# Kernel optimization log

Measured on AMD Instinct MI355X. Metric: run time of the kernel, lower is better.

Reference implementation:

```python
import jax, jax.numpy as jnp
import numpy as np

H = 128; NC = 100000; ND = 20000; NG = 50000; E = 150000; EP = 100000; L = 2

def _ln(x, g, b, eps=1e-5):
    mu = jnp.mean(x, -1, keepdims=True)
    v = jnp.mean((x - mu) ** 2, -1, keepdims=True)
    return (x - mu) * jax.lax.rsqrt(v + eps) * g + b

def _gelu(x):
    return jax.nn.gelu(x, approximate=False)  # torch nn.GELU default = exact erf

def _sage(x_src, x_dst, ei, Wl, bl, Wr):
    # PyG SAGEConv: mean-aggregate src features over incoming edges, lin_l(agg)+bias + lin_r(x_dst)
    n_dst = x_dst.shape[0]
    msg = x_src[ei[0]]                                   # [E, H] gather
    s = jax.ops.segment_sum(msg, ei[1], num_segments=n_dst)
    cnt = jax.ops.segment_sum(jnp.ones((ei.shape[1],), x_src.dtype), ei[1], num_segments=n_dst)
    agg = s / jnp.maximum(cnt, 1.0)[:, None]             # zero for isolated dst nodes
    return agg @ Wl + bl + x_dst @ Wr

def _make_ei(k, ns, nd, e):
    k1, k2 = jax.random.split(k)
    return jnp.stack([jax.random.randint(k1, (e,), 0, ns, dtype=jnp.int32),
                      jax.random.randint(k2, (e,), 0, nd, dtype=jnp.int32)])

def setup_inputs() -> dict:
    key = jax.random.key(0)
    ks = jax.random.split(key, 16)
    s = 0.05
    return {
        "x_chem": jax.random.normal(ks[0], (NC, 128), jnp.float32),
        "x_dis": jax.random.normal(ks[1], (ND, 128), jnp.float32),
        "gene_emb": jax.random.normal(ks[2], (NG, H), jnp.float32) * s,
        "proj_W": jax.random.normal(ks[3], (2, 128, H), jnp.float32) * s,
        "proj_b": jnp.zeros((2, H), jnp.float32),
        "proj_ln_g": jnp.ones((2, H), jnp.float32),
        "proj_ln_b": jnp.zeros((2, H), jnp.float32),
        "sage_Wl": jax.random.normal(ks[4], (L, 4, H, H), jnp.float32) * s,
        "sage_bl": jnp.zeros((L, 4, H), jnp.float32),
        "sage_Wr": jax.random.normal(ks[5], (L, 4, H, H), jnp.float32) * s,
        "ln_g": jnp.ones((L, 3, H), jnp.float32),
        "ln_b": jnp.zeros((L, 3, H), jnp.float32),
        "W_cd": jax.random.normal(ks[6], (H, H), jnp.float32) * s,
        "ei_c2d": _make_ei(ks[7], NC, ND, E),
        "ei_d2c": _make_ei(ks[8], ND, NC, E),
        "ei_c2g": _make_ei(ks[9], NC, NG, E),
        "ei_g2c": _make_ei(ks[10], NG, NC, E),
        "pos_edge": _make_ei(ks[11], NC, ND, EP),
        "neg_edge": _make_ei(ks[12], NC, ND, EP),
    }

def reference(x_chem, x_dis, gene_emb, proj_W, proj_b, proj_ln_g, proj_ln_b,
              sage_Wl, sage_bl, sage_Wr, ln_g, ln_b, W_cd,
              ei_c2d, ei_d2c, ei_c2g, ei_g2c, pos_edge, neg_edge):
    # init node states: Linear+LN+GELU for featured ntypes, embedding table for gene
    hc = _gelu(_ln(x_chem @ proj_W[0] + proj_b[0], proj_ln_g[0], proj_ln_b[0]))
    hd = _gelu(_ln(x_dis @ proj_W[1] + proj_b[1], proj_ln_g[1], proj_ln_b[1]))
    hg = gene_emb
    for l in range(L):
        # HeteroConv aggr='mean': chemical receives d2c (idx1) and g2c (idx3) -> mean of 2
        nc = 0.5 * (_sage(hd, hc, ei_d2c, sage_Wl[l, 1], sage_bl[l, 1], sage_Wr[l, 1])
                    + _sage(hg, hc, ei_g2c, sage_Wl[l, 3], sage_bl[l, 3], sage_Wr[l, 3]))
        nd = _sage(hc, hd, ei_c2d, sage_Wl[l, 0], sage_bl[l, 0], sage_Wr[l, 0])
        ng = _sage(hc, hg, ei_c2g, sage_Wl[l, 2], sage_bl[l, 2], sage_Wr[l, 2])
        # residual + LN + GELU (dropout is identity in eval mode)
        hc = _gelu(_ln(nc + hc, ln_g[l, 0], ln_b[l, 0]))
        hd = _gelu(_ln(nd + hd, ln_g[l, 1], ln_b[l, 1]))
        hg = _gelu(_ln(ng + hg, ln_g[l, 2], ln_b[l, 2]))
    def dec(ei):
        return ((hc[ei[0]] @ W_cd) * hd[ei[1]]).sum(-1)
    return dec(pos_edge), dec(neg_edge)
```

## Files before the change

### kernel.cpp

```cpp
#include <hip/hip_runtime.h>

#define HD 128

constexpr int T_NC = 100000;
constexpr int T_ND = 20000;
constexpr int T_NG = 50000;
constexpr int T_E  = 150000;
constexpr int T_EP = 100000;
constexpr int NMAT = 21;
constexpr int DEGN = 2 * T_NC + T_ND + T_NG;

typedef __attribute__((ext_vector_type(8))) short   s16x8;
typedef __attribute__((ext_vector_type(8))) __bf16  bf16x8;
typedef __attribute__((ext_vector_type(4))) float   f32x4;

union Frag { s16x8 s; bf16x8 b; };

__device__ __forceinline__ float gelu_f(float x) {
    return 0.5f * x * (1.0f + erff(x * 0.70710678118654752f));
}

__global__ void pack_weights(const float* __restrict__ proj_W,
                             const float* __restrict__ sage_Wl,
                             const float* __restrict__ sage_Wr,
                             const float* __restrict__ W_cd,
                             unsigned short* __restrict__ phi,
                             unsigned short* __restrict__ plo)
{
    int m = blockIdx.x;
    const float* W;
    const float* W2 = nullptr;
    if (m < 2)        W = proj_W  + (size_t)m * HD * HD;
    else if (m < 10)  W = sage_Wl + (size_t)(m - 2) * HD * HD;
    else if (m < 18)  W = sage_Wr + (size_t)(m - 10) * HD * HD;
    else if (m == 18) W = W_cd;
    else {
        int l = m - 19;
        W  = sage_Wr + (size_t)(l * 4 + 1) * HD * HD;
        W2 = sage_Wr + (size_t)(l * 4 + 3) * HD * HD;
    }

    int t = threadIdx.x;
    int kstep = t >> 6;
    int lane  = t & 63;
    int kbase = kstep * 32 + (lane >> 4) * 8;
    int c     = lane & 15;
    for (int cb = 0; cb < 8; ++cb) {
        int col = cb * 16 + c;
        size_t off = ((((size_t)m * 8 + cb) * 4 + kstep) * 64 + lane) * 8;
        #pragma unroll
        for (int j = 0; j < 8; ++j) {
            float w = W[(size_t)(kbase + j) * HD + col];
            if (W2) w += W2[(size_t)(kbase + j) * HD + col];
            __bf16 h = (__bf16)w;
            union { __bf16 b; unsigned short u; } ch, cl;
            ch.b = h;
            cl.b = (__bf16)(w - (float)h);
            phi[off + j] = ch.u;
            plo[off + j] = cl.u;
        }
    }
}

__global__ void conv_gene(const float* __restrict__ src, unsigned short* __restrict__ dst)
{
    size_t i = (size_t)(blockIdx.x * blockDim.x + threadIdx.x) * 8;
    if (i >= (size_t)T_NG * HD) return;
    f32x4 a0 = *(const f32x4*)(src + i);
    f32x4 a1 = *(const f32x4*)(src + i + 4);
    Frag u;
    u.b[0] = (__bf16)a0.x; u.b[1] = (__bf16)a0.y; u.b[2] = (__bf16)a0.z; u.b[3] = (__bf16)a0.w;
    u.b[4] = (__bf16)a1.x; u.b[5] = (__bf16)a1.y; u.b[6] = (__bf16)a1.z; u.b[7] = (__bf16)a1.w;
    *(s16x8*)(dst + i) = u.s;
}

__global__ void edge_count4(const int* __restrict__ eA, const int* __restrict__ eB,
                            const int* __restrict__ eC, const int* __restrict__ eD,
                            int gPer, int* __restrict__ deg)
{
    int seg = blockIdx.x / gPer;
    int e = (blockIdx.x % gPer) * 256 + threadIdx.x;
    if (e >= T_E) return;
    const int* ei = seg == 0 ? eA : seg == 1 ? eB : seg == 2 ? eC : eD;
    int off = seg == 0 ? 0 : seg == 1 ? T_NC : seg == 2 ? 2 * T_NC : 2 * T_NC + T_ND;
    atomicAdd(&deg[off + ei[T_E + e]], 1);
}

__global__ void scan_local(const int* __restrict__ deg, int* __restrict__ rp,
                           int* __restrict__ bsum, int N)
{
    __shared__ int wtot[4];
    int t = threadIdx.x;
    int lane = t & 63, w = t >> 6;
    int base = blockIdx.x * 1024 + t * 4;
    int v[4];
    #pragma unroll
    for (int j = 0; j < 4; ++j) v[j] = (base + j < N) ? deg[base + j] : 0;
    int p1 = v[0] + v[1];
    int p2 = p1 + v[2];
    int total = p2 + v[3];
    int sc = total;
    #pragma unroll
    for (int o = 1; o < 64; o <<= 1) {
        int y = __shfl_up(sc, o);
        if (lane >= o) sc += y;
    }
    if (lane == 63) wtot[w] = sc;
    __syncthreads();
    int woff = 0;
    for (int i = 0; i < w; ++i) woff += wtot[i];
    int ex = woff + sc - total;
    if (base + 0 < N) rp[base + 0] = ex;
    if (base + 1 < N) rp[base + 1] = ex + v[0];
    if (base + 2 < N) rp[base + 2] = ex + p1;
    if (base + 3 < N) rp[base + 3] = ex + p2;
    if (t == 255) bsum[blockIdx.x] = woff + sc;
}

__global__ void scan_tops(int* __restrict__ bsum, int B)
{
    int lane = threadIdx.x;
    int off = 0;
    for (int s = 0; s < B; s += 64) {
        int i = s + lane;
        int v = (i < B) ? bsum[i] : 0;
        int sc = v;
        #pragma unroll
        for (int o = 1; o < 64; o <<= 1) {
            int y = __shfl_up(sc, o);
            if (lane >= o) sc += y;
        }
        if (i < B) bsum[i] = off + sc - v;
        off += __shfl(sc, 63);
    }
}

__global__ void scan_add(int* __restrict__ rp, const int* __restrict__ bsum, int N)
{
    int base = blockIdx.x * 1024 + threadIdx.x * 4;
    int o = bsum[blockIdx.x];
    #pragma unroll
    for (int j = 0; j < 4; ++j)
        if (base + j < N) rp[base + j] += o;
}

__global__ void edge_fill4(const int* __restrict__ eA, const int* __restrict__ eB,
                           const int* __restrict__ eC, const int* __restrict__ eD,
                           int gPer, const int* __restrict__ rp,
                           int* __restrict__ fil, int* __restrict__ col)
{
    int seg = blockIdx.x / gPer;
    int e = (blockIdx.x % gPer) * 256 + threadIdx.x;
    if (e >= T_E) return;
    const int* ei = seg == 0 ? eA : seg == 1 ? eB : seg == 2 ? eC : eD;
    int off = seg == 0 ? 0 : seg == 1 ? T_NC : seg == 2 ? 2 * T_NC : 2 * T_NC + T_ND;
    int d = ei[T_E + e];
    int p = rp[off + d] + atomicAdd(&fil[off + d], 1);
    col[p] = ei[e];
}

struct Pair {
    const void* A;
    const int* rp; const int* dg; const int* col;
    int w; int fmt;
};
struct Seg {
    Pair p0, p1, p2;
    const float *bias0, *bias1, *g_ln, *b_ln;
    unsigned short* out;
    float scale;
    int np, use_res, M, nblk;
};

template<int MODE>
__global__ __launch_bounds__(256, 8)
void fused_gemm(Seg s0, Seg s1, Seg s2,
                const unsigned short* __restrict__ phi,
                const unsigned short* __restrict__ plo)
{
    __shared__ __align__(16) unsigned short As_hi[32 * HD];
    __shared__ __align__(16) unsigned short As_lo[32 * HD];
    __shared__ float psum[4][32];
    __shared__ float psq[4][32];

    int bid = blockIdx.x;
    Seg s;
    if (bid < s0.nblk) s = s0;
    else if (bid < s0.nblk + s1.nblk) { bid -= s0.nblk; s = s1; }
    else { bid -= s0.nblk + s1.nblk; s = s2; }

    const int tid  = threadIdx.x;
    const int w    = tid >> 6;
    const int lane = tid & 63;
    const int c    = lane & 15;
    const int hi4  = lane >> 4;
    const int row0 = bid * 32;

    f32x4 acc[2][2];
    #pragma unroll
    for (int rb = 0; rb < 2; ++rb)
        #pragma unroll
        for (int q = 0; q < 2; ++q) acc[rb][q] = (f32x4)0.f;

    for (int p = 0; p < s.np; ++p) {
        Pair P = (p == 0) ? s.p0 : (p == 1) ? s.p1 : s.p2;
        const bool gath = (P.rp != nullptr);

        __syncthreads();
        for (int it = 0; it < 2; ++it) {
            int u  = tid + it * 256;
            int r  = u >> 4;
            int k8 = (u & 15) * 8;
            int gr = row0 + r;
            Frag vh, vl;
            vh.s = (s16x8)0; vl.s = (s16x8)0;
            if (gr < s.M) {
                if (gath) {
                    float av[8] = {0.f, 0.f, 0.f, 0.f, 0.f, 0.f, 0.f, 0.f};
                    int st = P.rp[gr];
                    int d  = P.dg[gr];
                    const unsigned short* Ah = (const unsigned short*)P.A;
                    int i = 0;
                    for (; i + 2 <= d; i += 2) {
                        int e0 = P.col[st + i];
                        int e1 = P.col[st + i + 1];
                        Frag x0, x1;
                        x0.s = *(const s16x8*)(Ah + (size_t)e0 * HD + k8);
                        x1.s = *(const s16x8*)(Ah + (size_t)e1 * HD + k8);
                        #pragma unroll
                        for (int j = 0; j < 8; ++j)
                            av[j] += (float)x0.b[j] + (float)x1.b[j];
                    }
                    if (i < d) {
                        int e0 = P.col[st + i];
                        Frag x0;
                        x0.s = *(const s16x8*)(Ah + (size_t)e0 * HD + k8);
                        #pragma unroll
                        for (int j = 0; j < 8; ++j)
                            av[j] += (float)x0.b[j];
                    }
                    float rs = 1.f / (float)(d > 1 ? d : 1);
                    #pragma unroll
                    for (int j = 0; j < 8; ++j) {
                        float x = av[j] * rs;
                        __bf16 h = (__bf16)x;
                        vh.b[j] = h;
                        vl.b[j] = (__bf16)(x - (float)h);
                    }
                } else if (P.fmt) {
                    vh.s = *(const s16x8*)((const unsigned short*)P.A + (size_t)gr * HD + k8);
                } else {
                    const f32x4* ap = (const f32x4*)((const float*)P.A + (size_t)gr * HD + k8);
                    f32x4 a0 = ap[0], a1 = ap[1];
                    vh.b[0] = (__bf16)a0.x; vh.b[1] = (__bf16)a0.y;
                    vh.b[2] = (__bf16)a0.z; vh.b[3] = (__bf16)a0.w;
                    vh.b[4] = (__bf16)a1.x; vh.b[5] = (__bf16)a1.y;
                    vh.b[6] = (__bf16)a1.z; vh.b[7] = (__bf16)a1.w;
                }
            }
            int sidx = (r * HD + k8) ^ ((r & 7) << 3);
            *(s16x8*)(As_hi + sidx) = vh.s;
            if (gath) *(s16x8*)(As_lo + sidx) = vl.s;
        }
        __syncthreads();

        #pragma unroll
        for (int ks = 0; ks < 4; ++ks) {
            Frag bh[2], bl[2];
            #pragma unroll
            for (int q = 0; q < 2; ++q) {
                int cbG = w * 2 + q;
                size_t boff = ((((size_t)P.w * 8 + cbG) * 4 + ks) * 64 + lane) * 8;
                bh[q].s = *(const s16x8*)(phi + boff);
                bl[q].s = *(const s16x8*)(plo + boff);
            }
            #pragma unroll
            for (int rb = 0; rb < 2; ++rb) {
                int r = rb * 16 + c;
                int sidx = (r * HD + ks * 32 + hi4 * 8) ^ ((r & 7) << 3);
                Frag ah;
                ah.s = *(const s16x8*)(As_hi + sidx);
                #pragma unroll
                for (int q = 0; q < 2; ++q) {
                    acc[rb][q] = __builtin_amdgcn_mfma_f32_16x16x32_bf16(ah.b, bh[q].b, acc[rb][q], 0, 0, 0);
                    acc[rb][q] = __builtin_amdgcn_mfma_f32_16x16x32_bf16(ah.b, bl[q].b, acc[rb][q], 0, 0, 0);
                }
                if (gath) {
                    Frag al;
                    al.s = *(const s16x8*)(As_lo + sidx);
                    #pragma unroll
                    for (int q = 0; q < 2; ++q)
                        acc[rb][q] = __builtin_amdgcn_mfma_f32_16x16x32_bf16(al.b, bh[q].b, acc[rb][q], 0, 0, 0);
                }
            }
        }
    }

    if (MODE == 0) {
        __syncthreads();
        #pragma unroll
        for (int rb = 0; rb < 2; ++rb)
            #pragma unroll
            for (int q = 0; q < 2; ++q) {
                int col = (w * 2 + q) * 16 + c;
                #pragma unroll
                for (int reg = 0; reg < 4; ++reg) {
                    int row = rb * 16 + hi4 * 4 + reg;
                    union { __bf16 b; unsigned short u; } cv;
                    cv.b = (__bf16)acc[rb][q][reg];
                    As_hi[row * HD + col] = cv.u;
                }
            }
        __syncthreads();
        int row = tid >> 3;
        int c8  = (tid & 7) * 8;
        int gr  = row0 + row;
        if (gr < s.M) {
            *(s16x8*)(s.out + (size_t)gr * HD + c8)      = *(const s16x8*)(As_hi + row * HD + c8);
            *(s16x8*)(s.out + (size_t)gr * HD + 64 + c8) = *(const s16x8*)(As_hi + row * HD + 64 + c8);
        }
        return;
    }

    float bsum_[2], gl[2], bb[2];
    #pragma unroll
    for (int q = 0; q < 2; ++q) {
        int col = (w * 2 + q) * 16 + c;
        float b = 0.f;
        if (s.bias0) b += s.bias0[col];
        if (s.bias1) b += s.bias1[col];
        bsum_[q] = b;
        gl[q] = s.g_ln[col];
        bb[q] = s.b_ln[col];
    }

    float v[2][2][4];
    #pragma unroll
    for (int rb = 0; rb < 2; ++rb)
        #pragma unroll
        for (int q = 0; q < 2; ++q) {
            int col = (w * 2 + q) * 16 + c;
            #pragma unroll
            for (int reg = 0; reg < 4; ++reg) {
                int row = rb * 16 + hi4 * 4 + reg;
                float r_ = 0.f;
                if (s.use_res) {
                    int sx = (row * HD + col) ^ ((row & 7) << 3);
                    union { unsigned short u; } t; t.u = As_hi[sx];
                    union { __bf16 b; unsigned short u; } cb; cb.u = t.u;
                    r_ = (float)cb.b;
                }
                v[rb][q][reg] = (acc[rb][q][reg] + bsum_[q]) * s.scale + r_;
            }
        }

    #pragma unroll
    for (int rb = 0; rb < 2; ++rb)
        #pragma unroll
        for (int reg = 0; reg < 4; ++reg) {
            float sm = v[rb][0][reg] + v[rb][1][reg];
            float qq = v[rb][0][reg] * v[rb][0][reg] + v[rb][1][reg] * v[rb][1][reg];
            #pragma unroll
            for (int m = 1; m <= 8; m <<= 1) {
                sm += __shfl_xor(sm, m);
                qq += __shfl_xor(qq, m);
            }
            if (c == 0) {
                int row = rb * 16 + hi4 * 4 + reg;
                psum[w][row] = sm;
                psq[w][row]  = qq;
            }
        }
    __syncthreads();

    #pragma unroll
    for (int rb = 0; rb < 2; ++rb)
        #pragma unroll
        for (int reg = 0; reg < 4; ++reg) {
            int row = rb * 16 + hi4 * 4 + reg;
            float S  = psum[0][row] + psum[1][row] + psum[2][row] + psum[3][row];
            float Q  = psq[0][row]  + psq[1][row]  + psq[2][row]  + psq[3][row];
            float mean = S * (1.f / 128.f);
            float var  = Q * (1.f / 128.f) - mean * mean;
            float rstd = rsqrtf(var + 1e-5f);
            #pragma unroll
            for (int q = 0; q < 2; ++q) {
                int col = (w * 2 + q) * 16 + c;
                float t = (v[rb][q][reg] - mean) * rstd * gl[q] + bb[q];
                union { __bf16 b; unsigned short u; } cv;
                cv.b = (__bf16)gelu_f(t);
                As_hi[row * HD + col] = cv.u;
            }
        }
    __syncthreads();

    {
        int row = tid >> 3;
        int c8  = (tid & 7) * 8;
        int gr  = row0 + row;
        if (gr < s.M) {
            *(s16x8*)(s.out + (size_t)gr * HD + c8)      = *(const s16x8*)(As_hi + row * HD + c8);
            *(s16x8*)(s.out + (size_t)gr * HD + 64 + c8) = *(const s16x8*)(As_hi + row * HD + 64 + c8);
        }
    }
}

__global__ void edge_score2(const int* __restrict__ pos, const int* __restrict__ neg,
                            const unsigned short* __restrict__ Pb,
                            const unsigned short* __restrict__ Hb,
                            float* __restrict__ out)
{
    int t = blockIdx.x * blockDim.x + threadIdx.x;
    int e = t >> 4;
    if (e >= 2 * T_EP) return;
    int lane = t & 15;
    const int* ei = pos;
    float* o = out;
    if (e >= T_EP) { e -= T_EP; ei = neg; o = out + T_EP; }
    int sI = ei[e];
    int dI = ei[T_EP + e];
    Frag p, h;
    p.s = *(const s16x8*)(Pb + (size_t)sI * HD + lane * 8);
    h.s = *(const s16x8*)(Hb + (size_t)dI * HD + lane * 8);
    float acc = 0.f;
    #pragma unroll
    for (int j = 0; j < 8; ++j)
        acc += (float)p.b[j] * (float)h.b[j];
    #pragma unroll
    for (int m = 1; m <= 8; m <<= 1) acc += __shfl_xor(acc, m);
    if (lane == 0) o[e] = acc;
}

extern "C" void kernel_launch(void* const* d_in, const int* in_sizes, int n_in,
                              void* d_out, int out_size, void* d_ws, size_t ws_size,
                              hipStream_t stream)
{
    const float* x_chem    = (const float*)d_in[0];
    const float* x_dis     = (const float*)d_in[1];
    const float* gene_emb  = (const float*)d_in[2];
    const float* proj_W    = (const float*)d_in[3];
    const float* proj_b    = (const float*)d_in[4];
    const float* proj_ln_g = (const float*)d_in[5];
    const float* proj_ln_b = (const float*)d_in[6];
    const float* sage_Wl   = (const float*)d_in[7];
    const float* sage_bl   = (const float*)d_in[8];
    const float* sage_Wr   = (const float*)d_in[9];
    const float* ln_g      = (const float*)d_in[10];
    const float* ln_b      = (const float*)d_in[11];
    const float* W_cd      = (const float*)d_in[12];
    const int*   ei_c2d    = (const int*)d_in[13];
    const int*   ei_d2c    = (const int*)d_in[14];
    const int*   ei_c2g    = (const int*)d_in[15];
    const int*   ei_g2c    = (const int*)d_in[16];
    const int*   pos_edge  = (const int*)d_in[17];
    const int*   neg_edge  = (const int*)d_in[18];
    float* out = (float*)d_out;

    unsigned short* us = (unsigned short*)d_ws;
    const size_t SC = (size_t)T_NC * HD, SD = (size_t)T_ND * HD, SG = (size_t)T_NG * HD;
    unsigned short* hc0  = us;
    unsigned short* hc1  = hc0 + SC;
    unsigned short* hd0  = hc1 + SC;
    unsigned short* hd1  = hd0 + SD;
    unsigned short* hgA  = hd1 + SD;
    unsigned short* hgB  = hgA + SG;
    unsigned short* geneB = hgB + SG;
    unsigned short* packHi = geneB + SG;
    unsigned short* packLo = packHi + (size_t)NMAT * HD * HD;
    int* ib  = (int*)(packLo + (size_t)NMAT * HD * HD);
    int* deg = ib;
    int* fil = deg + DEGN;
    int* rp  = fil + DEGN;
    int* col = rp + DEGN;
    int* bsum = col + 4 * T_E;
    unsigned short* Pb = hc1;

    const dim3 blk(256);
    const int gC = (T_NC + 31) / 32;
    const int gD = (T_ND + 31) / 32;
    const int gG = (T_NG + 31) / 32;
    const int gE256 = (T_E + 255) / 256;
    const int gScan = (DEGN + 1023) / 1024;
    const int gConv = (int)(((size_t)T_NG * HD / 8 + 255) / 256);
    const int OFF_DC = 0, OFF_GC = T_NC, OFF_CD = 2 * T_NC, OFF_CG = 2 * T_NC + T_ND;

    pack_weights<<<NMAT, blk, 0, stream>>>(proj_W, sage_Wl, sage_Wr, W_cd, packHi, packLo);
    conv_gene<<<gConv, blk, 0, stream>>>(gene_emb, geneB);
    hipMemsetAsync(deg, 0, (size_t)2 * DEGN * sizeof(int), stream);

    edge_count4<<<4 * gE256, blk, 0, stream>>>(ei_d2c, ei_g2c, ei_c2d, ei_c2g, gE256, deg);
    scan_local<<<gScan, blk, 0, stream>>>(deg, rp, bsum, DEGN);
    scan_tops<<<1, 64, 0, stream>>>(bsum, gScan);
    scan_add<<<gScan, blk, 0, stream>>>(rp, bsum, DEGN);
    edge_fill4<<<4 * gE256, blk, 0, stream>>>(ei_d2c, ei_g2c, ei_c2d, ei_c2g, gE256, rp, fil, col);

    Seg z{};

    {
        Seg pc{};
        pc.p0.A = x_chem; pc.p0.w = 0; pc.p0.fmt = 0;
        pc.np = 1; pc.use_res = 0;
        pc.bias0 = proj_b; pc.g_ln = proj_ln_g; pc.b_ln = proj_ln_b;
        pc.scale = 1.f; pc.out = hc0; pc.M = T_NC; pc.nblk = gC;
        Seg pd{};
        pd.p0.A = x_dis; pd.p0.w = 1; pd.p0.fmt = 0;
        pd.np = 1; pd.use_res = 0;
        pd.bias0 = proj_b + HD; pd.g_ln = proj_ln_g + HD; pd.b_ln = proj_ln_b + HD;
        pd.scale = 1.f; pd.out = hd0; pd.M = T_ND; pd.nblk = gD;
        fused_gemm<1><<<gC + gD, blk, 0, stream>>>(pc, pd, z, packHi, packLo);
    }

    for (int l = 0; l < 2; ++l) {
        const float* bl = sage_bl + (size_t)l * 4 * HD;
        const float* lg = ln_g + (size_t)l * 3 * HD;
        const float* lb = ln_b + (size_t)l * 3 * HD;
        const int wl = 2 + l * 4;
        const int wr = 10 + l * 4;
        const int wsum = 19 + l;

        const unsigned short* hcC = (l == 0) ? hc0 : hc1;
        unsigned short*       hcN = (l == 0) ? hc1 : hc0;
        const unsigned short* hdC = (l == 0) ? hd0 : hd1;
        unsigned short*       hdN = (l == 0) ? hd1 : hd0;
        const unsigned short* hgC = (l == 0) ? geneB : hgA;
        unsigned short*       hgN = (l == 0) ? hgA : hgB;

        Seg sc{};
        sc.p0.A = hdC; sc.p0.fmt = 1; sc.p0.rp = rp + OFF_DC; sc.p0.dg = deg + OFF_DC; sc.p0.col = col; sc.p0.w = wl + 1;
        sc.p1.A = hgC; sc.p1.fmt = 1; sc.p1.rp = rp + OFF_GC; sc.p1.dg = deg + OFF_GC; sc.p1.col = col; sc.p1.w = wl + 3;
        sc.p2.A = hcC; sc.p2.fmt = 1; sc.p2.w = wsum;
        sc.np = 3; sc.use_res = 1;
        sc.bias0 = bl + 1 * HD; sc.bias1 = bl + 3 * HD;
        sc.scale = 0.5f; sc.g_ln = lg; sc.b_ln = lb;
        sc.out = hcN; sc.M = T_NC; sc.nblk = gC;

        Seg sd{};
        sd.p0.A = hcC; sd.p0.fmt = 1; sd.p0.rp = rp + OFF_CD; sd.p0.dg = deg + OFF_CD; sd.p0.col = col; sd.p0.w = wl + 0;
        sd.p1.A = hdC; sd.p1.fmt = 1; sd.p1.w = wr + 0;
        sd.np = 2; sd.use_res = 1;
        sd.bias0 = bl + 0 * HD;
        sd.scale = 1.f; sd.g_ln = lg + HD; sd.b_ln = lb + HD;
        sd.out = hdN; sd.M = T_ND; sd.nblk = gD;

        Seg sg{};
        sg.p0.A = hcC; sg.p0.fmt = 1; sg.p0.rp = rp + OFF_CG; sg.p0.dg = deg + OFF_CG; sg.p0.col = col; sg.p0.w = wl + 2;
        sg.p1.A = hgC; sg.p1.fmt = 1; sg.p1.w = wr + 2;
        sg.np = 2; sg.use_res = 1;
        sg.bias0 = bl + 2 * HD;
        sg.scale = 1.f; sg.g_ln = lg + 2 * HD; sg.b_ln = lb + 2 * HD;
        sg.out = hgN; sg.M = T_NG; sg.nblk = gG;

        fused_gemm<1><<<gC + gD + gG, blk, 0, stream>>>(sc, sd, sg, packHi, packLo);
    }

    {
        Seg sp{};
        sp.p0.A = hc0; sp.p0.fmt = 1; sp.p0.w = 18;
        sp.np = 1; sp.use_res = 0;
        sp.scale = 1.f; sp.out = Pb; sp.M = T_NC; sp.nblk = gC;
        fused_gemm<0><<<gC, blk, 0, stream>>>(sp, z, z, packHi, packLo);
    }

    const int gEdge = (2 * T_EP * 16 + 255) / 256;
    edge_score2<<<gEdge, blk, 0, stream>>>(pos_edge, neg_edge, Pb, hd0, out);
}
```

Baseline: 406.9 us.

## Skip unused last-layer gene update, apply W_cd to disease side, interleave gathers

```diff
diff --git a/kernel.cpp b/kernel.cpp
--- a/kernel.cpp
+++ b/kernel.cpp
@@ -30,10 +30,11 @@
     int m = blockIdx.x;
     const float* W;
     const float* W2 = nullptr;
+    bool transp = false;
     if (m < 2)        W = proj_W  + (size_t)m * HD * HD;
     else if (m < 10)  W = sage_Wl + (size_t)(m - 2) * HD * HD;
     else if (m < 18)  W = sage_Wr + (size_t)(m - 10) * HD * HD;
-    else if (m == 18) W = W_cd;
+    else if (m == 18) { W = W_cd; transp = true; }
     else {
         int l = m - 19;
         W  = sage_Wr + (size_t)(l * 4 + 1) * HD * HD;
@@ -50,8 +51,9 @@
         size_t off = ((((size_t)m * 8 + cb) * 4 + kstep) * 64 + lane) * 8;
         #pragma unroll
         for (int j = 0; j < 8; ++j) {
-            float w = W[(size_t)(kbase + j) * HD + col];
-            if (W2) w += W2[(size_t)(kbase + j) * HD + col];
+            int k = kbase + j;
+            float w = transp ? W[(size_t)col * HD + k] : W[(size_t)k * HD + col];
+            if (W2) w += W2[(size_t)k * HD + col];
             __bf16 h = (__bf16)w;
             union { __bf16 b; unsigned short u; } ch, cl;
             ch.b = h;
@@ -172,6 +174,14 @@
     int np, use_res, M, nblk;
 };
 
+__device__ __forceinline__ void accum_row(const unsigned short* Ah, int e, int k8, float* av)
+{
+    Frag x;
+    x.s = *(const s16x8*)(Ah + (size_t)e * HD + k8);
+    #pragma unroll
+    for (int j = 0; j < 8; ++j) av[j] += (float)x.b[j];
+}
+
 template<int MODE>
 __global__ __launch_bounds__(256, 8)
 void fused_gemm(Seg s0, Seg s1, Seg s2,
@@ -202,65 +212,120 @@
         #pragma unroll
         for (int q = 0; q < 2; ++q) acc[rb][q] = (f32x4)0.f;
 
+    const int rS  = tid >> 4;
+    const int k8S = (tid & 15) * 8;
+    const int grA = row0 + rS;
+    const int grB = row0 + rS + 16;
+
     for (int p = 0; p < s.np; ++p) {
         Pair P = (p == 0) ? s.p0 : (p == 1) ? s.p1 : s.p2;
         const bool gath = (P.rp != nullptr);
 
         __syncthreads();
-        for (int it = 0; it < 2; ++it) {
-            int u  = tid + it * 256;
-            int r  = u >> 4;
-            int k8 = (u & 15) * 8;
-            int gr = row0 + r;
-            Frag vh, vl;
-            vh.s = (s16x8)0; vl.s = (s16x8)0;
-            if (gr < s.M) {
-                if (gath) {
-                    float av[8] = {0.f, 0.f, 0.f, 0.f, 0.f, 0.f, 0.f, 0.f};
-                    int st = P.rp[gr];
-                    int d  = P.dg[gr];
-                    const unsigned short* Ah = (const unsigned short*)P.A;
-                    int i = 0;
-                    for (; i + 2 <= d; i += 2) {
-                        int e0 = P.col[st + i];
-                        int e1 = P.col[st + i + 1];
-                        Frag x0, x1;
-                        x0.s = *(const s16x8*)(Ah + (size_t)e0 * HD + k8);
-                        x1.s = *(const s16x8*)(Ah + (size_t)e1 * HD + k8);
-                        #pragma unroll
-                        for (int j = 0; j < 8; ++j)
-                            av[j] += (float)x0.b[j] + (float)x1.b[j];
-                    }
-                    if (i < d) {
-                        int e0 = P.col[st + i];
-                        Frag x0;
-                        x0.s = *(const s16x8*)(Ah + (size_t)e0 * HD + k8);
-                        #pragma unroll
-                        for (int j = 0; j < 8; ++j)
-                            av[j] += (float)x0.b[j];
-                    }
-                    float rs = 1.f / (float)(d > 1 ? d : 1);
+        {
+            Frag vhA, vlA, vhB, vlB;
+            vhA.s = (s16x8)0; vlA.s = (s16x8)0;
+            vhB.s = (s16x8)0; vlB.s = (s16x8)0;
+            const bool vA = grA < s.M;
+            const bool vB = grB < s.M;
+            if (gath) {
+                const unsigned short* Ah = (const unsigned short*)P.A;
+                int stA = 0, dA = 0, stB = 0, dB = 0;
+                if (vA) { stA = P.rp[grA]; dA = P.dg[grA]; }
+                if (vB) { stB = P.rp[grB]; dB = P.dg[grB]; }
+                float avA[8] = {0.f,0.f,0.f,0.f,0.f,0.f,0.f,0.f};
+                float avB[8] = {0.f,0.f,0.f,0.f,0.f,0.f,0.f,0.f};
+                int n = dA < dB ? dA : dB;
+                int i = 0;
+                for (; i + 2 <= n; i += 2) {
+                    int eA0 = P.col[stA + i],     eB0 = P.col[stB + i];
+                    int eA1 = P.col[stA + i + 1], eB1 = P.col[stB + i + 1];
+                    Frag xA0, xB0, xA1, xB1;
+                    xA0.s = *(const s16x8*)(Ah + (size_t)eA0 * HD + k8S);
+                    xB0.s = *(const s16x8*)(Ah + (size_t)eB0 * HD + k8S);
+                    xA1.s = *(const s16x8*)(Ah + (size_t)eA1 * HD + k8S);
+                    xB1.s = *(const s16x8*)(Ah + (size_t)eB1 * HD + k8S);
                     #pragma unroll
                     for (int j = 0; j < 8; ++j) {
-                        float x = av[j] * rs;
-                        __bf16 h = (__bf16)x;
-                        vh.b[j] = h;
-                        vl.b[j] = (__bf16)(x - (float)h);
+                        avA[j] += (float)xA0.b[j] + (float)xA1.b[j];
+                        avB[j] += (float)xB0.b[j] + (float)xB1.b[j];
                     }
-                } else if (P.fmt) {
-                    vh.s = *(const s16x8*)((const unsigned short*)P.A + (size_t)gr * HD + k8);
-                } else {
-                    const f32x4* ap = (const f32x4*)((const float*)P.A + (size_t)gr * HD + k8);
+                }
+                if (i < n) {
+                    int eA0 = P.col[stA + i], eB0 = P.col[stB + i];
+                    Frag xA0, xB0;
+                    xA0.s = *(const s16x8*)(Ah + (size_t)eA0 * HD + k8S);
+                    xB0.s = *(const s16x8*)(Ah + (size_t)eB0 * HD + k8S);
+                    #pragma unroll
+                    for (int j = 0; j < 8; ++j) {
+                        avA[j] += (float)xA0.b[j];
+                        avB[j] += (float)xB0.b[j];
+                    }
+                    ++i;
+                }
+                int iA = i;
+                for (; iA + 2 <= dA; iA += 2) {
+                    int e0 = P.col[stA + iA], e1 = P.col[stA + iA + 1];
+                    Frag x0, x1;
+                    x0.s = *(const s16x8*)(Ah + (size_t)e0 * HD + k8S);
+                    x1.s = *(const s16x8*)(Ah + (size_t)e1 * HD + k8S);
+                    #pragma unroll
+                    for (int j = 0; j < 8; ++j) avA[j] += (float)x0.b[j] + (float)x1.b[j];
+                }
+                if (iA < dA) accum_row(Ah, P.col[stA + iA], k8S, avA);
+                int iB = i;
+                for (; iB + 2 <= dB; iB += 2) {
+                    int e0 = P.col[stB + iB], e1 = P.col[stB + iB + 1];
+                    Frag x0, x1;
+                    x0.s = *(const s16x8*)(Ah + (size_t)e0 * HD + k8S);
+                    x1.s = *(const s16x8*)(Ah + (size_t)e1 * HD + k8S);
+                    #pragma unroll
+                    for (int j = 0; j < 8; ++j) avB[j] += (float)x0.b[j] + (float)x1.b[j];
+                }
+                if (iB < dB) accum_row(Ah, P.col[stB + iB], k8S, avB);
+
+                float rsA = 1.f / (float)(dA > 1 ? dA : 1);
+                float rsB = 1.f / (float)(dB > 1 ? dB : 1);
+                #pragma unroll
+                for (int j = 0; j < 8; ++j) {
+                    float xa = avA[j] * rsA;
+                    __bf16 ha = (__bf16)xa;
+                    vhA.b[j] = ha; vlA.b[j] = (__bf16)(xa - (float)ha);
+                    float xb = avB[j] * rsB;
+                    __bf16 hb = (__bf16)xb;
+                    vhB.b[j] = hb; vlB.b[j] = (__bf16)(xb - (float)hb);
+                }
+            } else if (P.fmt) {
+                const unsigned short* Ah = (const unsigned short*)P.A;
+                if (vA) vhA.s = *(const s16x8*)(Ah + (size_t)grA * HD + k8S);
+                if (vB) vhB.s = *(const s16x8*)(Ah + (size_t)grB * HD + k8S);
+            } else {
+                const float* Af = (const float*)P.A;
+                if (vA) {
+                    const f32x4* ap = (const f32x4*)(Af + (size_t)grA * HD + k8S);
                     f32x4 a0 = ap[0], a1 = ap[1];
-                    vh.b[0] = (__bf16)a0.x; vh.b[1] = (__bf16)a0.y;
-                    vh.b[2] = (__bf16)a0.z; vh.b[3] = (__bf16)a0.w;
-                    vh.b[4] = (__bf16)a1.x; vh.b[5] = (__bf16)a1.y;
-                    vh.b[6] = (__bf16)a1.z; vh.b[7] = (__bf16)a1.w;
-                }
-            }
-            int sidx = (r * HD + k8) ^ ((r & 7) << 3);
-            *(s16x8*)(As_hi + sidx) = vh.s;
-            if (gath) *(s16x8*)(As_lo + sidx) = vl.s;
+                    vhA.b[0] = (__bf16)a0.x; vhA.b[1] = (__bf16)a0.y;
+                    vhA.b[2] = (__bf16)a0.z; vhA.b[3] = (__bf16)a0.w;
+                    vhA.b[4] = (__bf16)a1.x; vhA.b[5] = (__bf16)a1.y;
+                    vhA.b[6] = (__bf16)a1.z; vhA.b[7] = (__bf16)a1.w;
+                }
+                if (vB) {
+                    const f32x4* bp = (const f32x4*)(Af + (size_t)grB * HD + k8S);
+                    f32x4 b0 = bp[0], b1 = bp[1];
+                    vhB.b[0] = (__bf16)b0.x; vhB.b[1] = (__bf16)b0.y;
+                    vhB.b[2] = (__bf16)b0.z; vhB.b[3] = (__bf16)b0.w;
+                    vhB.b[4] = (__bf16)b1.x; vhB.b[5] = (__bf16)b1.y;
+                    vhB.b[6] = (__bf16)b1.z; vhB.b[7] = (__bf16)b1.w;
+                }
+            }
+            int sA = (rS * HD + k8S) ^ ((rS & 7) << 3);
+            int sB = ((rS + 16) * HD + k8S) ^ ((rS & 7) << 3);
+            *(s16x8*)(As_hi + sA) = vhA.s;
+            *(s16x8*)(As_hi + sB) = vhB.s;
+            if (gath) {
+                *(s16x8*)(As_lo + sA) = vlA.s;
+                *(s16x8*)(As_lo + sB) = vlB.s;
+            }
         }
         __syncthreads();
 
@@ -312,12 +377,12 @@
                 }
             }
         __syncthreads();
-        int row = tid >> 3;
-        int c8  = (tid & 7) * 8;
-        int gr  = row0 + row;
-        if (gr < s.M) {
-            *(s16x8*)(s.out + (size_t)gr * HD + c8)      = *(const s16x8*)(As_hi + row * HD + c8);
-            *(s16x8*)(s.out + (size_t)gr * HD + 64 + c8) = *(const s16x8*)(As_hi + row * HD + 64 + c8);
+        #pragma unroll
+        for (int it2 = 0; it2 < 2; ++it2) {
+            int rr = rS + it2 * 16;
+            int gr = row0 + rr;
+            if (gr < s.M)
+                *(s16x8*)(s.out + (size_t)gr * HD + k8S) = *(const s16x8*)(As_hi + rr * HD + k8S);
         }
         return;
     }
@@ -346,8 +411,7 @@
                 float r_ = 0.f;
                 if (s.use_res) {
                     int sx = (row * HD + col) ^ ((row & 7) << 3);
-                    union { unsigned short u; } t; t.u = As_hi[sx];
-                    union { __bf16 b; unsigned short u; } cb; cb.u = t.u;
+                    union { __bf16 b; unsigned short u; } cb; cb.u = As_hi[sx];
                     r_ = (float)cb.b;
                 }
                 v[rb][q][reg] = (acc[rb][q][reg] + bsum_[q]) * s.scale + r_;
@@ -394,20 +458,18 @@
         }
     __syncthreads();
 
-    {
-        int row = tid >> 3;
-        int c8  = (tid & 7) * 8;
-        int gr  = row0 + row;
-        if (gr < s.M) {
-            *(s16x8*)(s.out + (size_t)gr * HD + c8)      = *(const s16x8*)(As_hi + row * HD + c8);
-            *(s16x8*)(s.out + (size_t)gr * HD + 64 + c8) = *(const s16x8*)(As_hi + row * HD + 64 + c8);
-        }
+    #pragma unroll
+    for (int it2 = 0; it2 < 2; ++it2) {
+        int rr = rS + it2 * 16;
+        int gr = row0 + rr;
+        if (gr < s.M)
+            *(s16x8*)(s.out + (size_t)gr * HD + k8S) = *(const s16x8*)(As_hi + rr * HD + k8S);
     }
 }
 
 __global__ void edge_score2(const int* __restrict__ pos, const int* __restrict__ neg,
-                            const unsigned short* __restrict__ Pb,
-                            const unsigned short* __restrict__ Hb,
+                            const unsigned short* __restrict__ Hc,
+                            const unsigned short* __restrict__ Qb,
                             float* __restrict__ out)
 {
     int t = blockIdx.x * blockDim.x + threadIdx.x;
@@ -420,8 +482,8 @@
     int sI = ei[e];
     int dI = ei[T_EP + e];
     Frag p, h;
-    p.s = *(const s16x8*)(Pb + (size_t)sI * HD + lane * 8);
-    h.s = *(const s16x8*)(Hb + (size_t)dI * HD + lane * 8);
+    p.s = *(const s16x8*)(Hc + (size_t)sI * HD + lane * 8);
+    h.s = *(const s16x8*)(Qb + (size_t)dI * HD + lane * 8);
     float acc = 0.f;
     #pragma unroll
     for (int j = 0; j < 8; ++j)
@@ -473,7 +535,7 @@
     int* rp  = fil + DEGN;
     int* col = rp + DEGN;
     int* bsum = col + 4 * T_E;
-    unsigned short* Pb = hc1;
+    unsigned short* Qb = hd1;
 
     const dim3 blk(256);
     const int gC = (T_NC + 31) / 32;
@@ -523,7 +585,7 @@
         const unsigned short* hdC = (l == 0) ? hd0 : hd1;
         unsigned short*       hdN = (l == 0) ? hd1 : hd0;
         const unsigned short* hgC = (l == 0) ? geneB : hgA;
-        unsigned short*       hgN = (l == 0) ? hgA : hgB;
+        unsigned short*       hgN = hgA;
 
         Seg sc{};
         sc.p0.A = hdC; sc.p0.fmt = 1; sc.p0.rp = rp + OFF_DC; sc.p0.dg = deg + OFF_DC; sc.p0.col = col; sc.p0.w = wl + 1;
@@ -542,25 +604,28 @@
         sd.scale = 1.f; sd.g_ln = lg + HD; sd.b_ln = lb + HD;
         sd.out = hdN; sd.M = T_ND; sd.nblk = gD;
 
-        Seg sg{};
-        sg.p0.A = hcC; sg.p0.fmt = 1; sg.p0.rp = rp + OFF_CG; sg.p0.dg = deg + OFF_CG; sg.p0.col = col; sg.p0.w = wl + 2;
-        sg.p1.A = hgC; sg.p1.fmt = 1; sg.p1.w = wr + 2;
-        sg.np = 2; sg.use_res = 1;
-        sg.bias0 = bl + 2 * HD;
-        sg.scale = 1.f; sg.g_ln = lg + 2 * HD; sg.b_ln = lb + 2 * HD;
-        sg.out = hgN; sg.M = T_NG; sg.nblk = gG;
-
-        fused_gemm<1><<<gC + gD + gG, blk, 0, stream>>>(sc, sd, sg, packHi, packLo);
+        if (l == 0) {
+            Seg sg{};
+            sg.p0.A = hcC; sg.p0.fmt = 1; sg.p0.rp = rp + OFF_CG; sg.p0.dg = deg + OFF_CG; sg.p0.col = col; sg.p0.w = wl + 2;
+            sg.p1.A = hgC; sg.p1.fmt = 1; sg.p1.w = wr + 2;
+            sg.np = 2; sg.use_res = 1;
+            sg.bias0 = bl + 2 * HD;
+            sg.scale = 1.f; sg.g_ln = lg + 2 * HD; sg.b_ln = lb + 2 * HD;
+            sg.out = hgN; sg.M = T_NG; sg.nblk = gG;
+            fused_gemm<1><<<gC + gD + gG, blk, 0, stream>>>(sc, sd, sg, packHi, packLo);
+        } else {
+            fused_gemm<1><<<gC + gD, blk, 0, stream>>>(sc, sd, z, packHi, packLo);
+        }
     }
 
     {
-        Seg sp{};
-        sp.p0.A = hc0; sp.p0.fmt = 1; sp.p0.w = 18;
-        sp.np = 1; sp.use_res = 0;
-        sp.scale = 1.f; sp.out = Pb; sp.M = T_NC; sp.nblk = gC;
-        fused_gemm<0><<<gC, blk, 0, stream>>>(sp, z, z, packHi, packLo);
+        Seg sq{};
+        sq.p0.A = hd0; sq.p0.fmt = 1; sq.p0.w = 18;
+        sq.np = 1; sq.use_res = 0;
+        sq.scale = 1.f; sq.out = Qb; sq.M = T_ND; sq.nblk = gD;
+        fused_gemm<0><<<gD, blk, 0, stream>>>(sq, z, z, packHi, packLo);
     }
 
     const int gEdge = (2 * T_EP * 16 + 255) / 256;
-    edge_score2<<<gEdge, blk, 0, stream>>>(pos_edge, neg_edge, Pb, hd0, out);
-}
+    edge_score2<<<gEdge, blk, 0, stream>>>(pos_edge, neg_edge, hc0, Qb, out);
+}
```

Result: slower. 476.5 us (+17.1%).

## Skip dead final gene-layer update and apply W_cd to disease side

Applied to the files above, without the earlier changes.

```diff
diff --git a/kernel.cpp b/kernel.cpp
--- a/kernel.cpp
+++ b/kernel.cpp
@@ -30,10 +30,11 @@
     int m = blockIdx.x;
     const float* W;
     const float* W2 = nullptr;
+    bool transp = false;
     if (m < 2)        W = proj_W  + (size_t)m * HD * HD;
     else if (m < 10)  W = sage_Wl + (size_t)(m - 2) * HD * HD;
     else if (m < 18)  W = sage_Wr + (size_t)(m - 10) * HD * HD;
-    else if (m == 18) W = W_cd;
+    else if (m == 18) { W = W_cd; transp = true; }
     else {
         int l = m - 19;
         W  = sage_Wr + (size_t)(l * 4 + 1) * HD * HD;
@@ -50,8 +51,9 @@
         size_t off = ((((size_t)m * 8 + cb) * 4 + kstep) * 64 + lane) * 8;
         #pragma unroll
         for (int j = 0; j < 8; ++j) {
-            float w = W[(size_t)(kbase + j) * HD + col];
-            if (W2) w += W2[(size_t)(kbase + j) * HD + col];
+            int k = kbase + j;
+            float w = transp ? W[(size_t)col * HD + k] : W[(size_t)k * HD + col];
+            if (W2) w += W2[(size_t)k * HD + col];
             __bf16 h = (__bf16)w;
             union { __bf16 b; unsigned short u; } ch, cl;
             ch.b = h;
@@ -346,8 +348,7 @@
                 float r_ = 0.f;
                 if (s.use_res) {
                     int sx = (row * HD + col) ^ ((row & 7) << 3);
-                    union { unsigned short u; } t; t.u = As_hi[sx];
-                    union { __bf16 b; unsigned short u; } cb; cb.u = t.u;
+                    union { __bf16 b; unsigned short u; } cb; cb.u = As_hi[sx];
                     r_ = (float)cb.b;
                 }
                 v[rb][q][reg] = (acc[rb][q][reg] + bsum_[q]) * s.scale + r_;
@@ -406,8 +407,8 @@
 }
 
 __global__ void edge_score2(const int* __restrict__ pos, const int* __restrict__ neg,
-                            const unsigned short* __restrict__ Pb,
-                            const unsigned short* __restrict__ Hb,
+                            const unsigned short* __restrict__ Hc,
+                            const unsigned short* __restrict__ Qb,
                             float* __restrict__ out)
 {
     int t = blockIdx.x * blockDim.x + threadIdx.x;
@@ -420,8 +421,8 @@
     int sI = ei[e];
     int dI = ei[T_EP + e];
     Frag p, h;
-    p.s = *(const s16x8*)(Pb + (size_t)sI * HD + lane * 8);
-    h.s = *(const s16x8*)(Hb + (size_t)dI * HD + lane * 8);
+    p.s = *(const s16x8*)(Hc + (size_t)sI * HD + lane * 8);
+    h.s = *(const s16x8*)(Qb + (size_t)dI * HD + lane * 8);
     float acc = 0.f;
     #pragma unroll
     for (int j = 0; j < 8; ++j)
@@ -473,7 +474,7 @@
     int* rp  = fil + DEGN;
     int* col = rp + DEGN;
     int* bsum = col + 4 * T_E;
-    unsigned short* Pb = hc1;
+    unsigned short* Qb = hd1;
 
     const dim3 blk(256);
     const int gC = (T_NC + 31) / 32;
@@ -523,7 +524,6 @@
         const unsigned short* hdC = (l == 0) ? hd0 : hd1;
         unsigned short*       hdN = (l == 0) ? hd1 : hd0;
         const unsigned short* hgC = (l == 0) ? geneB : hgA;
-        unsigned short*       hgN = (l == 0) ? hgA : hgB;
 
         Seg sc{};
         sc.p0.A = hdC; sc.p0.fmt = 1; sc.p0.rp = rp + OFF_DC; sc.p0.dg = deg + OFF_DC; sc.p0.col = col; sc.p0.w = wl + 1;
@@ -542,25 +542,28 @@
         sd.scale = 1.f; sd.g_ln = lg + HD; sd.b_ln = lb + HD;
         sd.out = hdN; sd.M = T_ND; sd.nblk = gD;
 
-        Seg sg{};
-        sg.p0.A = hcC; sg.p0.fmt = 1; sg.p0.rp = rp + OFF_CG; sg.p0.dg = deg + OFF_CG; sg.p0.col = col; sg.p0.w = wl + 2;
-        sg.p1.A = hgC; sg.p1.fmt = 1; sg.p1.w = wr + 2;
-        sg.np = 2; sg.use_res = 1;
-        sg.bias0 = bl + 2 * HD;
-        sg.scale = 1.f; sg.g_ln = lg + 2 * HD; sg.b_ln = lb + 2 * HD;
-        sg.out = hgN; sg.M = T_NG; sg.nblk = gG;
-
-        fused_gemm<1><<<gC + gD + gG, blk, 0, stream>>>(sc, sd, sg, packHi, packLo);
+        if (l == 0) {
+            Seg sg{};
+            sg.p0.A = hcC; sg.p0.fmt = 1; sg.p0.rp = rp + OFF_CG; sg.p0.dg = deg + OFF_CG; sg.p0.col = col; sg.p0.w = wl + 2;
+            sg.p1.A = hgC; sg.p1.fmt = 1; sg.p1.w = wr + 2;
+            sg.np = 2; sg.use_res = 1;
+            sg.bias0 = bl + 2 * HD;
+            sg.scale = 1.f; sg.g_ln = lg + 2 * HD; sg.b_ln = lb + 2 * HD;
+            sg.out = hgA; sg.M = T_NG; sg.nblk = gG;
+            fused_gemm<1><<<gC + gD + gG, blk, 0, stream>>>(sc, sd, sg, packHi, packLo);
+        } else {
+            fused_gemm<1><<<gC + gD, blk, 0, stream>>>(sc, sd, z, packHi, packLo);
+        }
     }
 
     {
-        Seg sp{};
-        sp.p0.A = hc0; sp.p0.fmt = 1; sp.p0.w = 18;
-        sp.np = 1; sp.use_res = 0;
-        sp.scale = 1.f; sp.out = Pb; sp.M = T_NC; sp.nblk = gC;
-        fused_gemm<0><<<gC, blk, 0, stream>>>(sp, z, z, packHi, packLo);
+        Seg sq{};
+        sq.p0.A = hd0; sq.p0.fmt = 1; sq.p0.w = 18;
+        sq.np = 1; sq.use_res = 0;
+        sq.scale = 1.f; sq.out = Qb; sq.M = T_ND; sq.nblk = gD;
+        fused_gemm<0><<<gD, blk, 0, stream>>>(sq, z, z, packHi, packLo);
     }
 
     const int gEdge = (2 * T_EP * 16 + 255) / 256;
-    edge_score2<<<gEdge, blk, 0, stream>>>(pos_edge, neg_edge, Pb, hd0, out);
-}
+    edge_score2<<<gEdge, blk, 0, stream>>>(pos_edge, neg_edge, hc0, Qb, out);
+}
```

Result: faster. 362.3 us (median of 2 runs) (-11.0%).
